# Optimization experiments

Hardware: AMD Instinct MI355X
Metric: run time of the kernel (lower is better)

The kernel has to match this reference:

```python
import jax, jax.numpy as jnp
import numpy as np

T, B, D, H = 512, 64, 1024, 1024


def setup_inputs() -> dict:
    key = jax.random.key(0)
    ks = jax.random.split(key, 9)
    s_in = 1.0 / np.sqrt(D + H)
    inp = {"x": jax.random.normal(ks[0], (T, B, D), dtype=jnp.float32)}
    names = ["f", "i", "g", "o"]
    for j, n in enumerate(names):
        inp[f"W{n}"] = jax.random.uniform(ks[1 + 2 * j], (D + H, H), jnp.float32, -s_in, s_in)
        inp[f"b{n}"] = jax.random.uniform(ks[2 + 2 * j], (H,), jnp.float32, -s_in, s_in)
    return inp


def reference(x, Wf, bf, Wi, bi, Wg, bg, Wo, bo):
    # Fuse the four gate GEMMs into one: [D+H, 4H]
    W = jnp.concatenate([Wf, Wi, Wg, Wo], axis=1)
    b = jnp.concatenate([bf, bi, bg, bo], axis=0)
    h0 = jnp.zeros((x.shape[1], H), dtype=x.dtype)
    c0 = jnp.zeros((x.shape[1], H), dtype=x.dtype)

    def step(carry, x_t):
        hx, cx = carry
        comb = jnp.concatenate([x_t, hx], axis=1)           # [B, D+H]
        gates = comb @ W + b                                 # [B, 4H]
        f = jax.nn.sigmoid(gates[:, 0 * H:1 * H])
        i = jax.nn.sigmoid(gates[:, 1 * H:2 * H])
        g = jnp.tanh(gates[:, 2 * H:3 * H])
        o = jax.nn.sigmoid(gates[:, 3 * H:4 * H])
        cx = f * cx + i * g
        hx = o * jnp.tanh(cx)
        return (hx, cx), hx

    (hT, cT), stacked = jax.lax.scan(step, (h0, c0), x)
    return stacked, (hT, cT)
```

## Files before the change

kernel.cpp:

```cpp
#include <hip/hip_runtime.h>
#include <hip/hip_bf16.h>
#include <stdint.h>


typedef unsigned short u16;
typedef __attribute__((ext_vector_type(8))) short s16x8;
typedef __attribute__((ext_vector_type(4))) float f32x4;

static constexpr int T_ = 512, B_ = 64, D_ = 1024, H_ = 1024;
static constexpr int MX_ = T_ * B_;
static constexpr int NG_ = 4 * H_;

__device__ __forceinline__ u16 f2bf(float f) {
  union { __hip_bfloat16 b; u16 u; } v;
  v.b = __float2bfloat16(f);
  return v.u;
}
__device__ __forceinline__ float bf2f(u16 u) {
  union { __hip_bfloat16 b; u16 u; } v;
  v.u = u;
  return __bfloat162float(v.b);
}

__device__ __forceinline__ void gload_lds16(const u16* g, u16* l) {
  __builtin_amdgcn_global_load_lds(
      (const __attribute__((address_space(1))) unsigned int*)(g),
      (__attribute__((address_space(3))) unsigned int*)(l), 16, 0, 0);
}

__device__ __forceinline__ float sigm(float x) {
  return __builtin_amdgcn_rcpf(1.f + __expf(-x));
}
__device__ __forceinline__ float tanh_(float x) {
  return 2.f * __builtin_amdgcn_rcpf(1.f + __expf(-2.f * x)) - 1.f;
}

__device__ __forceinline__ float gxload(const float* p) { return *p; }
__device__ __forceinline__ float gxload(const u16* p) { return bf2f(*p); }
__device__ __forceinline__ void gxstore(float* p, float v) { *p = v; }
__device__ __forceinline__ void gxstore(u16* p, float v) { *p = f2bf(v); }

__global__ __launch_bounds__(256) void k_cast_x(const float* __restrict__ x,
                                                u16* __restrict__ xb) {
  size_t i = ((size_t)blockIdx.x * 256 + threadIdx.x) * 8;
  const float4* xp = (const float4*)(x + i);
  float4 a = xp[0], b = xp[1];
  s16x8 o;
  o[0] = (short)f2bf(a.x); o[1] = (short)f2bf(a.y);
  o[2] = (short)f2bf(a.z); o[3] = (short)f2bf(a.w);
  o[4] = (short)f2bf(b.x); o[5] = (short)f2bf(b.y);
  o[6] = (short)f2bf(b.z); o[7] = (short)f2bf(b.w);
  *(s16x8*)(xb + i) = o;
}

__global__ __launch_bounds__(256) void k_prep_w(
    const float* __restrict__ Wf, const float* __restrict__ Wi,
    const float* __restrict__ Wg, const float* __restrict__ Wo,
    const float* __restrict__ bf_, const float* __restrict__ bi_,
    const float* __restrict__ bg_, const float* __restrict__ bo_,
    u16* __restrict__ wxt, u16* __restrict__ whr, float* __restrict__ biasf) {
  const int bid = blockIdx.x;
  const int t = threadIdx.x;
  const float* Ws[4] = {Wf, Wi, Wg, Wo};
  {
    const float* src = Ws[bid >> 10];
    const int col = bid & 1023;
#pragma unroll
    for (int it = 0; it < 4; ++it) {
      int k = t + it * 256;
      wxt[(size_t)bid * 1024 + k] = f2bf(src[(size_t)k * 1024 + col]);
    }
  }
  {
    const int g = bid >> 6, c = bid & 63;
    const float* src = Ws[c & 3];
    const int col = g * 16 + ((c >> 4) << 2) + ((c >> 2) & 3);
#pragma unroll
    for (int it = 0; it < 4; ++it) {
      int k = t + it * 256;
      whr[(size_t)bid * 1024 + k] = f2bf(src[(size_t)(1024 + k) * 1024 + col]);
    }
  }
  if (t == 0) {
    const float* bs[4] = {bf_, bi_, bg_, bo_};
    biasf[bid] = bs[bid >> 10][bid & 1023];
  }
}

template <typename GT>
__global__ __launch_bounds__(256) void k_gemm_gx(
    const u16* __restrict__ A,
    const u16* __restrict__ Bt,
    const float* __restrict__ biasf,
    GT* __restrict__ C) {
  __shared__ u16 aLds[128 * 32];
  __shared__ u16 bLds[128 * 32];
  const int tid = threadIdx.x;
  const int w = tid >> 6, l = tid & 63;
  const int q = l >> 4, cc = l & 15;
  const int bm = blockIdx.x, bn = blockIdx.y;
  const int wm = (w & 1) * 64, wn = (w >> 1) * 64;
  const int lrow = l >> 2, lchunk = (l & 3) * 8;

  f32x4 zero = {0.f, 0.f, 0.f, 0.f};
  f32x4 acc[4][4];
#pragma unroll
  for (int i = 0; i < 4; ++i)
#pragma unroll
    for (int j = 0; j < 4; ++j) acc[i][j] = zero;

  for (int k0 = 0; k0 < 1024; k0 += 32) {
#pragma unroll
    for (int r = 0; r < 2; ++r) {
      gload_lds16(A + (size_t)(bm * 128 + r * 64 + w * 16 + lrow) * 1024 + k0 + lchunk,
                  &aLds[(r * 64 + w * 16) * 32]);
      gload_lds16(Bt + (size_t)(bn * 128 + r * 64 + w * 16 + lrow) * 1024 + k0 + lchunk,
                  &bLds[(r * 64 + w * 16) * 32]);
    }
    __syncthreads();
    s16x8 af[4], bf[4];
#pragma unroll
    for (int i = 0; i < 4; ++i)
      af[i] = *(const s16x8*)&aLds[(wm + i * 16 + cc) * 32 + q * 8];
#pragma unroll
    for (int j = 0; j < 4; ++j)
      bf[j] = *(const s16x8*)&bLds[(wn + j * 16 + cc) * 32 + q * 8];
#pragma unroll
    for (int i = 0; i < 4; ++i)
#pragma unroll
      for (int j = 0; j < 4; ++j)
        acc[i][j] = __builtin_amdgcn_mfma_f32_16x16x32_bf16(af[i], bf[j], acc[i][j], 0, 0, 0);
    __syncthreads();
  }
#pragma unroll
  for (int i = 0; i < 4; ++i) {
    const int row0 = bm * 128 + wm + i * 16 + q * 4;
#pragma unroll
    for (int j = 0; j < 4; ++j) {
      const int col = bn * 128 + wn + j * 16 + cc;
      const float bb = biasf[col];
#pragma unroll
      for (int r = 0; r < 4; ++r)
        gxstore(C + (size_t)(row0 + r) * 4096 + col, acc[i][j][r] + bb);
    }
  }
}

template <typename GT>
__global__ __launch_bounds__(256, 1) void k_lstm(
    const u16* __restrict__ Whr,
    const GT* __restrict__ Gx,
    u16* __restrict__ hbuf,
    float* __restrict__ out,
    unsigned* __restrict__ flags) {
  __shared__ s16x8 wl[32 * 4 * 64];
  __shared__ u16 hl[16 * 1024];
  const int tid = threadIdx.x;
  const int w = tid >> 6, l = tid & 63, q = l >> 4, cc = l & 15;
  const int m = blockIdx.x >> 6, g = blockIdx.x & 63;
  const int gate = cc & 3;
  const int hcol = g * 16 + w * 4 + (cc >> 2);
  const int gxcol = gate * 1024 + hcol;
  const int wcol = w * 16 + cc;
  unsigned* gflag = flags + m * (64 * 32);

  {
    const int col = tid >> 2;
    const int kb = (tid & 3) * 256;
    const u16* src = Whr + (size_t)(g * 64 + col) * 1024 + kb;
#pragma unroll
    for (int i = 0; i < 8; ++i) {
      const int kk = kb / 32 + i;
#pragma unroll
      for (int qq = 0; qq < 4; ++qq)
        wl[(kk * 4 + qq) * 64 + col] = *(const s16x8*)(src + i * 32 + qq * 8);
    }
  }

  const int xb = (cc >> 2) & 1;
  const u16* hb0 = hl + cc * 1024 + ((q ^ (cc & 3)) + 4 * xb) * 8;
  const u16* hb1 = hl + cc * 1024 + ((q ^ (cc & 3)) + 4 * (1 - xb)) * 8;

  auto refill = [&](int buf) {
    const u16* hsrc = hbuf + (size_t)buf * (B_ * H_) + (size_t)m * 16 * 1024;
    unsigned long long vb[16];
#pragma unroll
    for (int s = 0; s < 8; ++s) {
      const int c = s * 256 + tid;
      const int r = c >> 7, p = c & 127;
      const unsigned long long* src =
          (const unsigned long long*)(hsrc + r * 1024 + (p ^ (r & 7)) * 8);
      vb[2 * s] = __hip_atomic_load(src, __ATOMIC_RELAXED, __HIP_MEMORY_SCOPE_AGENT);
      vb[2 * s + 1] =
          __hip_atomic_load(src + 1, __ATOMIC_RELAXED, __HIP_MEMORY_SCOPE_AGENT);
    }
#pragma unroll
    for (int s = 0; s < 8; ++s) {
      union { unsigned long long u[2]; s16x8 v; } t2;
      t2.u[0] = vb[2 * s]; t2.u[1] = vb[2 * s + 1];
      *(s16x8*)(hl + (s * 256 + tid) * 8) = t2.v;
    }
  };

  float cst[4] = {0.f, 0.f, 0.f, 0.f};
  float hlast[4] = {0.f, 0.f, 0.f, 0.f};

  float gxv[4];
  {
    const GT* gp = Gx + (size_t)(m * 16 + q * 4) * 4096 + gxcol;
#pragma unroll
    for (int r = 0; r < 4; ++r) gxv[r] = gxload(gp + (size_t)r * 4096);
  }

  refill(0);
  __syncthreads();

#define BFRAG(kk) (wl[((kk) * 4 + q) * 64 + wcol])

  int polldead = 0;

  for (int t = 0; t < T_; ++t) {
    f32x4 acc0 = {0.f, 0.f, 0.f, 0.f}, acc1 = {0.f, 0.f, 0.f, 0.f};
#pragma unroll
    for (int I = 0; I < 32; I += 2) {
      s16x8 a0 = *(const s16x8*)(hb0 + (I >> 1) * 64);
      s16x8 a1 = *(const s16x8*)(hb1 + (I >> 1) * 64);
      acc0 = __builtin_amdgcn_mfma_f32_16x16x32_bf16(a0, BFRAG(I), acc0, 0, 0, 0);
      acc1 = __builtin_amdgcn_mfma_f32_16x16x32_bf16(a1, BFRAG(I + 1), acc1, 0, 0, 0);
    }

    float v0[4];
#pragma unroll
    for (int r = 0; r < 4; ++r) {
      float x = acc0[r] + acc1[r] + gxv[r];
      v0[r] = (gate == 2) ? tanh_(x) : sigm(x);
    }
#pragma unroll
    for (int r = 0; r < 4; ++r) {
      float a0 = v0[r];
      float a1 = __shfl_xor(a0, 1);
      float a2 = __shfl_xor(a0, 2);
      float a3 = __shfl_xor(a1, 2);
      float fv = (gate == 0) ? a0 : (gate == 1) ? a1 : (gate == 2) ? a2 : a3;
      float iv = (gate == 0) ? a1 : (gate == 1) ? a0 : (gate == 2) ? a3 : a2;
      float gv = (gate == 0) ? a2 : (gate == 1) ? a3 : (gate == 2) ? a0 : a1;
      float ov = (gate == 0) ? a3 : (gate == 1) ? a2 : (gate == 2) ? a1 : a0;
      float cn = fv * cst[r] + iv * gv;
      cst[r] = cn;
      hlast[r] = ov * tanh_(cn);
    }

    if (gate == 0) {
      u16* hd = hbuf + (size_t)((t + 1) & 1) * (B_ * H_);
#pragma unroll
      for (int r = 0; r < 4; ++r) {
        const int row = m * 16 + q * 4 + r;
        __hip_atomic_store(hd + row * 1024 + hcol, f2bf(hlast[r]),
                           __ATOMIC_RELAXED, __HIP_MEMORY_SCOPE_AGENT);
      }
    }
    __syncthreads();
    if (tid == 0)
      __hip_atomic_store(&gflag[g * 32], (unsigned)(t + 1), __ATOMIC_RELAXED,
                         __HIP_MEMORY_SCOPE_AGENT);
    asm volatile("" ::: "memory");

    float gxn[4];
    {
      const int tn = (t + 1) & 511;
      const GT* gp = Gx + (size_t)(tn * 64 + m * 16 + q * 4) * 4096 + gxcol;
#pragma unroll
      for (int r = 0; r < 4; ++r) gxn[r] = gxload(gp + (size_t)r * 4096);
    }
    if (gate == 0) {
#pragma unroll
      for (int r = 0; r < 4; ++r) {
        const int row = m * 16 + q * 4 + r;
        out[(size_t)(t * 64 + row) * 1024 + hcol] = hlast[r];
      }
    }

    if (w == 0 && !polldead) {
      const unsigned* fp = gflag + l * 32;
      for (unsigned it = 0;; ++it) {
        unsigned v = __hip_atomic_load(fp, __ATOMIC_RELAXED,
                                       __HIP_MEMORY_SCOPE_AGENT);
        if (__all(v > (unsigned)t)) break;
        if (it > (1u << 22)) { polldead = 1; break; }
        __builtin_amdgcn_s_sleep(1);
      }
    }
    __syncthreads();

    refill((t + 1) & 1);
    __syncthreads();

#pragma unroll
    for (int r = 0; r < 4; ++r) gxv[r] = gxn[r];
  }
#undef BFRAG

  if (gate == 0) {
    float* hT = out + (size_t)T_ * B_ * H_;
    float* cT = hT + B_ * H_;
#pragma unroll
    for (int r = 0; r < 4; ++r) {
      const int row = m * 16 + q * 4 + r;
      hT[row * 1024 + hcol] = hlast[r];
      cT[row * 1024 + hcol] = cst[r];
    }
  }
}

extern "C" void kernel_launch(void* const* d_in, const int* in_sizes, int n_in,
                              void* d_out, int out_size, void* d_ws, size_t ws_size,
                              hipStream_t stream) {
  (void)in_sizes; (void)n_in; (void)out_size;
  const float* x   = (const float*)d_in[0];
  const float* Wf  = (const float*)d_in[1];
  const float* bf_ = (const float*)d_in[2];
  const float* Wi  = (const float*)d_in[3];
  const float* bi_ = (const float*)d_in[4];
  const float* Wg  = (const float*)d_in[5];
  const float* bg_ = (const float*)d_in[6];
  const float* Wo  = (const float*)d_in[7];
  const float* bo_ = (const float*)d_in[8];
  float* out = (float*)d_out;

  uint8_t* ws = (uint8_t*)d_ws;
  const size_t n_gx    = (size_t)MX_ * NG_;
  const size_t sz_xb   = (size_t)MX_ * 1024 * 2;
  const size_t sz_wxt  = (size_t)4096 * 1024 * 2;
  const size_t sz_whr  = (size_t)4096 * 1024 * 2;
  const size_t sz_bias = 4096 * 4;
  const size_t sz_hbuf = (size_t)2 * 64 * 1024 * 2;
  const size_t sz_ctrl = 4 * 64 * 32 * 4 + 8192;
  const size_t fixed = sz_xb + sz_wxt + sz_whr + sz_bias + sz_hbuf + sz_ctrl + 1024;
  const bool f32gx = ws_size >= fixed + n_gx * 4;
  const size_t sz_gx = n_gx * (f32gx ? 4 : 2);

  size_t off = 0;
  uint8_t* p_gx   = ws;                  off += sz_gx;
  u16*     xb     = (u16*)(ws + off);    off += sz_xb;
  u16*     wxt    = (u16*)(ws + off);    off += sz_wxt;
  u16*     whr    = (u16*)(ws + off);    off += sz_whr;
  float*   biasf  = (float*)(ws + off);  off += sz_bias;
  u16*     hbuf   = (u16*)(ws + off);    off += sz_hbuf;
  unsigned* flags = (unsigned*)(ws + off);

  hipMemsetAsync(hbuf, 0, sz_hbuf + sz_ctrl, stream);
  k_cast_x<<<(MX_ * 1024) / (256 * 8), 256, 0, stream>>>(x, xb);
  k_prep_w<<<4096, 256, 0, stream>>>(Wf, Wi, Wg, Wo, bf_, bi_, bg_, bo_, wxt, whr, biasf);
  if (f32gx) {
    k_gemm_gx<float><<<dim3(256, 32), 256, 0, stream>>>(xb, wxt, biasf, (float*)p_gx);
    k_lstm<float><<<256, 256, 0, stream>>>(whr, (const float*)p_gx, hbuf, out, flags);
  } else {
    k_gemm_gx<u16><<<dim3(256, 32), 256, 0, stream>>>(xb, wxt, biasf, (u16*)p_gx);
    k_lstm<u16><<<256, 256, 0, stream>>>(whr, (const u16*)p_gx, hbuf, out, flags);
  }
}
```

Measured before the change: 2.444 ms.

## Keep recurrent weights in registers, double-buffer h in LDS, drop barriers

Recurrent weight fragments now live in 32 VGPR vectors per lane instead of LDS, freeing LDS for a double-buffered h tile. With two h buffers, the barrier between polling and refill is removed and every wave polls the flags itself. The final step skips the h store, flag update and refill, and the poll timeout is shortened. This cuts per-step LDS traffic and one or two block-wide barriers on the serial critical path, at the cost of 128 extra VGPRs per lane (pressure or spills) and more polling traffic from all four waves.

```diff
diff --git a/kernel.cpp b/kernel.cpp
--- a/kernel.cpp
+++ b/kernel.cpp
@@ -4,6 +4,8 @@
 
 
 typedef unsigned short u16;
+typedef unsigned int u32;
+typedef unsigned long long u64;
 typedef __attribute__((ext_vector_type(8))) short s16x8;
 typedef __attribute__((ext_vector_type(4))) float f32x4;
 
@@ -153,8 +155,7 @@
     u16* __restrict__ hbuf,
     float* __restrict__ out,
     unsigned* __restrict__ flags) {
-  __shared__ s16x8 wl[32 * 4 * 64];
-  __shared__ u16 hl[16 * 1024];
+  __shared__ u16 hl[2 * 16 * 1024];
   const int tid = threadIdx.x;
   const int w = tid >> 6, l = tid & 63, q = l >> 4, cc = l & 15;
   const int m = blockIdx.x >> 6, g = blockIdx.x & 63;
@@ -164,41 +165,36 @@
   const int wcol = w * 16 + cc;
   unsigned* gflag = flags + m * (64 * 32);
 
+  s16x8 bfr[32];
   {
-    const int col = tid >> 2;
-    const int kb = (tid & 3) * 256;
-    const u16* src = Whr + (size_t)(g * 64 + col) * 1024 + kb;
-#pragma unroll
-    for (int i = 0; i < 8; ++i) {
-      const int kk = kb / 32 + i;
-#pragma unroll
-      for (int qq = 0; qq < 4; ++qq)
-        wl[(kk * 4 + qq) * 64 + col] = *(const s16x8*)(src + i * 32 + qq * 8);
-    }
-  }
-
-  const int xb = (cc >> 2) & 1;
-  const u16* hb0 = hl + cc * 1024 + ((q ^ (cc & 3)) + 4 * xb) * 8;
-  const u16* hb1 = hl + cc * 1024 + ((q ^ (cc & 3)) + 4 * (1 - xb)) * 8;
+    const u16* src = Whr + (size_t)(g * 64 + wcol) * 1024 + q * 8;
+#pragma unroll
+    for (int kk = 0; kk < 32; ++kk)
+      bfr[kk] = *(const s16x8*)(src + kk * 32);
+  }
+
+  const int xbit = (cc >> 2) & 1;
+  const int off0 = cc * 1024 + ((q ^ (cc & 3)) + 4 * xbit) * 8;
+  const int off1 = cc * 1024 + ((q ^ (cc & 3)) + 4 * (1 - xbit)) * 8;
 
   auto refill = [&](int buf) {
     const u16* hsrc = hbuf + (size_t)buf * (B_ * H_) + (size_t)m * 16 * 1024;
-    unsigned long long vb[16];
+    u64 vb[16];
 #pragma unroll
     for (int s = 0; s < 8; ++s) {
       const int c = s * 256 + tid;
       const int r = c >> 7, p = c & 127;
-      const unsigned long long* src =
-          (const unsigned long long*)(hsrc + r * 1024 + (p ^ (r & 7)) * 8);
+      const u64* src = (const u64*)(hsrc + r * 1024 + (p ^ (r & 7)) * 8);
       vb[2 * s] = __hip_atomic_load(src, __ATOMIC_RELAXED, __HIP_MEMORY_SCOPE_AGENT);
       vb[2 * s + 1] =
           __hip_atomic_load(src + 1, __ATOMIC_RELAXED, __HIP_MEMORY_SCOPE_AGENT);
     }
+    u16* dst = hl + buf * (16 * 1024);
 #pragma unroll
     for (int s = 0; s < 8; ++s) {
-      union { unsigned long long u[2]; s16x8 v; } t2;
+      union { u64 u[2]; s16x8 v; } t2;
       t2.u[0] = vb[2 * s]; t2.u[1] = vb[2 * s + 1];
-      *(s16x8*)(hl + (s * 256 + tid) * 8) = t2.v;
+      *(s16x8*)(dst + (s * 256 + tid) * 8) = t2.v;
     }
   };
 
@@ -215,18 +211,17 @@
   refill(0);
   __syncthreads();
 
-#define BFRAG(kk) (wl[((kk) * 4 + q) * 64 + wcol])
-
   int polldead = 0;
 
   for (int t = 0; t < T_; ++t) {
+    const u16* hbase = hl + (t & 1) * (16 * 1024);
     f32x4 acc0 = {0.f, 0.f, 0.f, 0.f}, acc1 = {0.f, 0.f, 0.f, 0.f};
 #pragma unroll
     for (int I = 0; I < 32; I += 2) {
-      s16x8 a0 = *(const s16x8*)(hb0 + (I >> 1) * 64);
-      s16x8 a1 = *(const s16x8*)(hb1 + (I >> 1) * 64);
-      acc0 = __builtin_amdgcn_mfma_f32_16x16x32_bf16(a0, BFRAG(I), acc0, 0, 0, 0);
-      acc1 = __builtin_amdgcn_mfma_f32_16x16x32_bf16(a1, BFRAG(I + 1), acc1, 0, 0, 0);
+      s16x8 a0 = *(const s16x8*)(hbase + off0 + (I >> 1) * 64);
+      s16x8 a1 = *(const s16x8*)(hbase + off1 + (I >> 1) * 64);
+      acc0 = __builtin_amdgcn_mfma_f32_16x16x32_bf16(a0, bfr[I], acc0, 0, 0, 0);
+      acc1 = __builtin_amdgcn_mfma_f32_16x16x32_bf16(a1, bfr[I + 1], acc1, 0, 0, 0);
     }
 
     float v0[4];
@@ -250,20 +245,24 @@
       hlast[r] = ov * tanh_(cn);
     }
 
-    if (gate == 0) {
-      u16* hd = hbuf + (size_t)((t + 1) & 1) * (B_ * H_);
-#pragma unroll
-      for (int r = 0; r < 4; ++r) {
-        const int row = m * 16 + q * 4 + r;
-        __hip_atomic_store(hd + row * 1024 + hcol, f2bf(hlast[r]),
-                           __ATOMIC_RELAXED, __HIP_MEMORY_SCOPE_AGENT);
+    const int nb = (t + 1) & 1;
+    const bool last = (t + 1 == T_);
+
+    if (!last) {
+      if (gate == 0) {
+        u16* hd = hbuf + (size_t)nb * (B_ * H_);
+#pragma unroll
+        for (int r = 0; r < 4; ++r) {
+          const int row = m * 16 + q * 4 + r;
+          __hip_atomic_store(hd + row * 1024 + hcol, f2bf(hlast[r]),
+                             __ATOMIC_RELAXED, __HIP_MEMORY_SCOPE_AGENT);
+        }
       }
-    }
-    __syncthreads();
-    if (tid == 0)
-      __hip_atomic_store(&gflag[g * 32], (unsigned)(t + 1), __ATOMIC_RELAXED,
-                         __HIP_MEMORY_SCOPE_AGENT);
-    asm volatile("" ::: "memory");
+      __syncthreads();
+      if (tid == 0)
+        __hip_atomic_store(&gflag[g * 32], (unsigned)(t + 1), __ATOMIC_RELAXED,
+                           __HIP_MEMORY_SCOPE_AGENT);
+    }
 
     float gxn[4];
     {
@@ -280,25 +279,25 @@
       }
     }
 
-    if (w == 0 && !polldead) {
-      const unsigned* fp = gflag + l * 32;
-      for (unsigned it = 0;; ++it) {
-        unsigned v = __hip_atomic_load(fp, __ATOMIC_RELAXED,
-                                       __HIP_MEMORY_SCOPE_AGENT);
-        if (__all(v > (unsigned)t)) break;
-        if (it > (1u << 22)) { polldead = 1; break; }
-        __builtin_amdgcn_s_sleep(1);
+    if (!last) {
+      if (!polldead) {
+        const unsigned* fp = gflag + l * 32;
+        for (unsigned it = 0;; ++it) {
+          unsigned v = __hip_atomic_load(fp, __ATOMIC_RELAXED,
+                                         __HIP_MEMORY_SCOPE_AGENT);
+          if (__all(v > (unsigned)t)) break;
+          if (it > (1u << 20)) { polldead = 1; break; }
+          __builtin_amdgcn_s_sleep(1);
+        }
       }
-    }
-    __syncthreads();
-
-    refill((t + 1) & 1);
-    __syncthreads();
+      asm volatile("" ::: "memory");
+      refill(nb);
+      __syncthreads();
+    }
 
 #pragma unroll
     for (int r = 0; r < 4; ++r) gxv[r] = gxn[r];
   }
-#undef BFRAG
 
   if (gate == 0) {
     float* hT = out + (size_t)T_ * B_ * H_;
@@ -334,7 +333,7 @@
   const size_t sz_whr  = (size_t)4096 * 1024 * 2;
   const size_t sz_bias = 4096 * 4;
   const size_t sz_hbuf = (size_t)2 * 64 * 1024 * 2;
-  const size_t sz_ctrl = 4 * 64 * 32 * 4 + 8192;
+  const size_t sz_ctrl = (size_t)4 * 64 * 32 * 4 + 8192;
   const size_t fixed = sz_xb + sz_wxt + sz_whr + sz_bias + sz_hbuf + sz_ctrl + 1024;
   const bool f32gx = ws_size >= fixed + n_gx * 4;
   const size_t sz_gx = n_gx * (f32gx ? 4 : 2);
```

Measured after the change: 2.355 ms. 3.6% less time.
